# Kernel optimization log

Measured on AMD Instinct MI355X. Metric: run time of the kernel, lower is better.

The kernel has to match this reference:

```python
import jax, jax.numpy as jnp
import numpy as np

B, L, C = 4, 16384, 512   # batch, tokens (128x128 grid), dim
NH, WS = 8, 8             # num_heads, window grid (ws)
HD = C // NH              # head_dim = 64


def setup_inputs() -> dict:
    key = jax.random.key(0)
    k1, k2, k3, k4, k5 = jax.random.split(key, 5)
    return {
        "q":   jax.random.normal(k1, (B, L, C), dtype=jnp.float32),
        "kv":  jax.random.normal(k2, (B, L, C), dtype=jnp.float32),
        "Wq":  jax.random.normal(k3, (C, C), dtype=jnp.float32) * 0.02,
        "Wkv": jax.random.normal(k4, (C, 2 * C), dtype=jnp.float32) * 0.02,
        "Wfc": jax.random.normal(k5, (C, C), dtype=jnp.float32) * 0.02,
    }


def reference(q, kv, Wq, Wkv, Wfc):
    Bq, Lq, Cd = q.shape
    Lkv = kv.shape[1]
    nh, hd, ws = NH, Cd // NH, WS
    scale = hd ** (-0.5)
    hw_q = int(round(Lq ** 0.5))   # 128
    hw_k = int(round(Lkv ** 0.5))
    sq, sk = hw_q // ws, hw_k // ws  # window side lengths (16)

    qp = q @ Wq                                   # [B, Lq, C]
    kvp = (kv @ Wkv).reshape(Bq, Lkv, 2, Cd)
    k, v = kvp[:, :, 0], kvp[:, :, 1]             # [B, Lkv, C]

    def window(x, s):
        # [B, hw, hw, C] -> [B, ws*ws windows, heads, s*s tokens, hd]
        x = x.reshape(Bq, ws, s, ws, s, Cd).transpose(0, 1, 3, 2, 4, 5)
        x = x.reshape(Bq, ws * ws, s * s, nh, hd)
        return x.transpose(0, 1, 3, 2, 4)

    qw = window(qp, sq)   # [B, W, H, sq*sq, hd]
    kw = window(k, sk)    # [B, W, H, sk*sk, hd]
    vw = window(v, sk)

    attn = jnp.einsum('bwhqd,bwhkd->bwhqk', qw, kw) * scale
    attn = jax.nn.softmax(attn, axis=-1)
    o = jnp.einsum('bwhqk,bwhkd->bwhqd', attn, vw)  # [B, W, H, sq*sq, hd]

    # inverse window partition
    o = o.transpose(0, 1, 3, 2, 4).reshape(Bq, ws, ws, sq, sq, Cd)
    o = o.transpose(0, 1, 3, 2, 4, 5).reshape(Bq, Lq, Cd)
    return o @ Wfc
```

## Files before the change

### kernel.cpp

```cpp
#include <hip/hip_runtime.h>
#include <stdint.h>

#define BB 4
#define LL 16384
#define CC 512
#define MM (BB * LL)

typedef unsigned short u16;
typedef __bf16 bf16x8 __attribute__((ext_vector_type(8)));
typedef float f32x4 __attribute__((ext_vector_type(4)));
typedef u16 u16x8 __attribute__((ext_vector_type(8)));
typedef u16 u16x4 __attribute__((ext_vector_type(4)));

__device__ __forceinline__ u16 f2bf(float f) {
  union { float f; uint32_t u; } c; c.f = f;
  return (u16)((c.u + 0x7fffu + ((c.u >> 16) & 1u)) >> 16);
}

__device__ __forceinline__ void gl_lds16(const void* g, void* l) {
  __builtin_amdgcn_global_load_lds((const __attribute__((address_space(1))) void*)g,
                                   (__attribute__((address_space(3))) void*)l,
                                   16, 0, 0);
}

__global__ void cvt_kernel(const float* __restrict__ in, u16* __restrict__ out, int n4) {
  for (int i = blockIdx.x * blockDim.x + threadIdx.x; i < n4; i += gridDim.x * blockDim.x) {
    float4 v = reinterpret_cast<const float4*>(in)[i];
    u16x4 o;
    o[0] = f2bf(v.x); o[1] = f2bf(v.y); o[2] = f2bf(v.z); o[3] = f2bf(v.w);
    reinterpret_cast<u16x4*>(out)[i] = o;
  }
}

__global__ void tcvt_kernel(const float* __restrict__ W, u16* __restrict__ Wt, int K, int N) {
  int idx = blockIdx.x * blockDim.x + threadIdx.x;
  if (idx >= K * N) return;
  int n = idx / K, k = idx % K;
  Wt[idx] = f2bf(W[k * N + n]);
}

template <bool OUT_F32>
__global__ __launch_bounds__(512, 2) void gemm256(const u16* __restrict__ A,
                                                  const u16* __restrict__ Bt,
                                                  void* __restrict__ Cp,
                                                  int M, int N, int K) {
  __shared__ __align__(16) u16 Al[2][16384];
  __shared__ __align__(16) u16 Bl[2][16384];
  const int nbn = N >> 8;
  const int nwg = gridDim.x;
  const int bid0 = blockIdx.x;
  const int cpx = nwg >> 3;
  const int bid = (bid0 & 7) * cpx + (bid0 >> 3);
  const int bm = bid / nbn, bn = bid % nbn;
  const size_t row0 = (size_t)bm << 8, col0 = (size_t)bn << 8;
  const int tid = threadIdx.x, lane = tid & 63;
  const int wv = tid >> 6, wm = wv >> 2, wn = wv & 3;
  const int ro = lane & 15, g4 = lane >> 4;
  const int NT = K >> 6;

  const int ci0 = tid, ci1 = tid + 512;
  const int r0 = ci0 >> 3, g0 = (ci0 & 7) ^ (r0 & 7);
  const int r1 = ci1 >> 3, g1 = (ci1 & 7) ^ (r1 & 7);

  auto stageA = [&](int half, int kt, u16* L) {
    gl_lds16(A + (row0 + half * 128 + r0) * (size_t)K + kt * 64 + g0 * 8, L + half * 8192 + ci0 * 8);
    gl_lds16(A + (row0 + half * 128 + r1) * (size_t)K + kt * 64 + g1 * 8, L + half * 8192 + ci1 * 8);
  };
  auto stageB = [&](int half, int kt, u16* L) {
    gl_lds16(Bt + (col0 + half * 128 + r0) * (size_t)K + kt * 64 + g0 * 8, L + half * 8192 + ci0 * 8);
    gl_lds16(Bt + (col0 + half * 128 + r1) * (size_t)K + kt * 64 + g1 * 8, L + half * 8192 + ci1 * 8);
  };

  const int aB = (wm * 128 + ro) * 64;
  const int bB = (wn * 64 + ro) * 64;
  const int sw0 = (g4 ^ (ro & 7)) * 8;
  const int sw1 = ((g4 + 4) ^ (ro & 7)) * 8;

  auto ldf = [&](const u16* p) { return *reinterpret_cast<const bf16x8*>(p); };

  f32x4 acc[8][4] = {};

  stageA(0, 0, Al[0]); stageA(1, 0, Al[0]); stageB(0, 0, Bl[0]); stageB(1, 0, Bl[0]);
  stageB(0, 1, Bl[1]); stageB(1, 1, Bl[1]);
  asm volatile("s_waitcnt vmcnt(4)" ::: "memory");
  __builtin_amdgcn_s_barrier();

  for (int t = 0; t < NT; t += 2) {
#pragma unroll
    for (int half = 0; half < 2; ++half) {
      const int u = t + half;
      u16* LA = Al[half];
      u16* LB = Bl[half];
      u16* LAn = Al[half ^ 1];
      const bool stA = (u + 1) < NT;
      const bool stB = (u + 2) < NT;
      bf16x8 bfr[4][2], af[2][2];

#pragma unroll
      for (int n = 0; n < 4; ++n) {
        bfr[n][0] = ldf(LB + bB + n * 1024 + sw0);
        bfr[n][1] = ldf(LB + bB + n * 1024 + sw1);
      }
      af[0][0] = ldf(LA + aB + sw0);        af[0][1] = ldf(LA + aB + sw1);
      af[1][0] = ldf(LA + aB + 1024 + sw0); af[1][1] = ldf(LA + aB + 1024 + sw1);
      if (stA) stageA(0, u + 1, LAn);
      __builtin_amdgcn_s_barrier();
      asm volatile("s_waitcnt lgkmcnt(0)" ::: "memory");
      __builtin_amdgcn_sched_barrier(0);
      __builtin_amdgcn_s_setprio(1);
#pragma unroll
      for (int m = 0; m < 2; ++m)
#pragma unroll
        for (int n = 0; n < 4; ++n) {
          acc[m][n] = __builtin_amdgcn_mfma_f32_16x16x32_bf16(af[m][0], bfr[n][0], acc[m][n], 0, 0, 0);
          acc[m][n] = __builtin_amdgcn_mfma_f32_16x16x32_bf16(af[m][1], bfr[n][1], acc[m][n], 0, 0, 0);
        }
      __builtin_amdgcn_s_setprio(0);
      __builtin_amdgcn_s_barrier();

#pragma unroll
      for (int ph = 1; ph < 4; ++ph) {
        af[0][0] = ldf(LA + aB + (2 * ph) * 1024 + sw0);
        af[0][1] = ldf(LA + aB + (2 * ph) * 1024 + sw1);
        af[1][0] = ldf(LA + aB + (2 * ph + 1) * 1024 + sw0);
        af[1][1] = ldf(LA + aB + (2 * ph + 1) * 1024 + sw1);
        if (ph == 1) { if (stA) stageA(1, u + 1, LAn); }
        else if (ph == 2) { if (stB) stageB(0, u + 2, LB); }
        else { if (stB) stageB(1, u + 2, LB); }
        __builtin_amdgcn_s_barrier();
        asm volatile("s_waitcnt lgkmcnt(0)" ::: "memory");
        __builtin_amdgcn_sched_barrier(0);
        __builtin_amdgcn_s_setprio(1);
#pragma unroll
        for (int m = 0; m < 2; ++m)
#pragma unroll
          for (int n = 0; n < 4; ++n) {
            acc[2 * ph + m][n] =
                __builtin_amdgcn_mfma_f32_16x16x32_bf16(af[m][0], bfr[n][0], acc[2 * ph + m][n], 0, 0, 0);
            acc[2 * ph + m][n] =
                __builtin_amdgcn_mfma_f32_16x16x32_bf16(af[m][1], bfr[n][1], acc[2 * ph + m][n], 0, 0, 0);
          }
        __builtin_amdgcn_s_setprio(0);
        if (ph == 3) {
          if (stB) asm volatile("s_waitcnt vmcnt(4)" ::: "memory");
          else     asm volatile("s_waitcnt vmcnt(0)" ::: "memory");
        }
        __builtin_amdgcn_s_barrier();
      }
    }
  }

#pragma unroll
  for (int m = 0; m < 8; ++m)
#pragma unroll
    for (int n = 0; n < 4; ++n)
#pragma unroll
      for (int j = 0; j < 4; ++j) {
        size_t r = row0 + wm * 128 + m * 16 + g4 * 4 + j;
        size_t c = col0 + wn * 64 + n * 16 + ro;
        if (OUT_F32)
          reinterpret_cast<float*>(Cp)[r * N + c] = acc[m][n][j];
        else
          reinterpret_cast<u16*>(Cp)[r * N + c] = f2bf(acc[m][n][j]);
      }
}

__global__ __launch_bounds__(512, 2) void attn_kernel(const u16* __restrict__ qp,
                                                      const u16* __restrict__ kvp,
                                                      u16* __restrict__ o) {
  __shared__ __align__(16) u16 Kl[256 * 72];
  __shared__ __align__(16) u16 Vt[64 * 264];
  __shared__ __align__(16) u16 Pl[8 * 16 * 264];
  const int bid = blockIdx.x;
  const int h = bid & 7, w = (bid >> 3) & 63, b = bid >> 9;
  const int w1 = w >> 3, w2 = w & 7;
  const int tid = threadIdx.x, lane = tid & 63, wv = tid >> 6;

  auto lrow = [&](int t) { return (w1 * 16 + (t >> 4)) * 128 + w2 * 16 + (t & 15); };

  {
    const int t = tid >> 1, half = tid & 1;
    const size_t base = ((size_t)(b * LL + lrow(t))) * 1024 + h * 64 + half * 32;
    const u16* kr = kvp + base;
    const u16* vr = kvp + base + 512;
#pragma unroll
    for (int c = 0; c < 4; ++c) {
      u16x8 kx = *reinterpret_cast<const u16x8*>(kr + c * 8);
      *reinterpret_cast<u16x8*>(&Kl[t * 72 + half * 32 + c * 8]) = kx;
    }
#pragma unroll
    for (int c = 0; c < 4; ++c) {
      u16x8 vx = *reinterpret_cast<const u16x8*>(vr + c * 8);
#pragma unroll
      for (int e = 0; e < 8; ++e) Vt[(half * 32 + c * 8 + e) * 264 + t] = vx[e];
    }
  }
  __syncthreads();

  const int ro = lane & 15;
  const int g4 = lane >> 4;
  const float scale = 0.125f;
  const int pbase = wv * 16 * 264;

#pragma unroll
  for (int rt = 0; rt < 2; ++rt) {
    const int tq = 32 * wv + 16 * rt + ro;
    const size_t qbase = ((size_t)(b * LL + lrow(tq))) * 512 + h * 64 + g4 * 8;
    const bf16x8 qf0 = *reinterpret_cast<const bf16x8*>(qp + qbase);
    const bf16x8 qf1 = *reinterpret_cast<const bf16x8*>(qp + qbase + 32);

    f32x4 sa[16] = {};
#pragma unroll
    for (int ct = 0; ct < 16; ++ct) {
      bf16x8 kf0 = *reinterpret_cast<const bf16x8*>(&Kl[(16 * ct + ro) * 72 + g4 * 8]);
      bf16x8 kf1 = *reinterpret_cast<const bf16x8*>(&Kl[(16 * ct + ro) * 72 + 32 + g4 * 8]);
      sa[ct] = __builtin_amdgcn_mfma_f32_16x16x32_bf16(qf0, kf0, sa[ct], 0, 0, 0);
      sa[ct] = __builtin_amdgcn_mfma_f32_16x16x32_bf16(qf1, kf1, sa[ct], 0, 0, 0);
    }

#pragma unroll
    for (int j = 0; j < 4; ++j) {
      float m = -1e30f;
#pragma unroll
      for (int ct = 0; ct < 16; ++ct) m = fmaxf(m, sa[ct][j]);
      m = fmaxf(m, __shfl_xor(m, 1));
      m = fmaxf(m, __shfl_xor(m, 2));
      m = fmaxf(m, __shfl_xor(m, 4));
      m = fmaxf(m, __shfl_xor(m, 8));
      m *= scale;
      float s = 0.f;
#pragma unroll
      for (int ct = 0; ct < 16; ++ct) {
        float p = __expf(sa[ct][j] * scale - m);
        sa[ct][j] = p;
        s += p;
      }
      s += __shfl_xor(s, 1);
      s += __shfl_xor(s, 2);
      s += __shfl_xor(s, 4);
      s += __shfl_xor(s, 8);
      float inv = 1.f / s;
#pragma unroll
      for (int ct = 0; ct < 16; ++ct)
        Pl[pbase + (g4 * 4 + j) * 264 + 16 * ct + ro] = f2bf(sa[ct][j] * inv);
    }

    f32x4 oacc[4] = {};
#pragma unroll
    for (int ks = 0; ks < 8; ++ks) {
      bf16x8 pf = *reinterpret_cast<const bf16x8*>(&Pl[pbase + ro * 264 + ks * 32 + g4 * 8]);
#pragma unroll
      for (int cd = 0; cd < 4; ++cd) {
        bf16x8 vf = *reinterpret_cast<const bf16x8*>(&Vt[(16 * cd + ro) * 264 + ks * 32 + g4 * 8]);
        oacc[cd] = __builtin_amdgcn_mfma_f32_16x16x32_bf16(pf, vf, oacc[cd], 0, 0, 0);
      }
    }

#pragma unroll
    for (int cd = 0; cd < 4; ++cd)
#pragma unroll
      for (int j = 0; j < 4; ++j) {
        int t = 32 * wv + 16 * rt + g4 * 4 + j;
        int d = 16 * cd + ro;
        o[((size_t)(b * LL + lrow(t))) * 512 + h * 64 + d] = f2bf(oacc[cd][j]);
      }
  }
}

extern "C" void kernel_launch(void* const* d_in, const int* in_sizes, int n_in,
                              void* d_out, int out_size, void* d_ws, size_t ws_size,
                              hipStream_t stream) {
  const float* q = (const float*)d_in[0];
  const float* kv = (const float*)d_in[1];
  const float* Wq = (const float*)d_in[2];
  const float* Wkv = (const float*)d_in[3];
  const float* Wfc = (const float*)d_in[4];
  float* out = (float*)d_out;
  char* ws = (char*)d_ws;

  u16* q_bf  = (u16*)(ws + 0);
  u16* kv_bf = (u16*)(ws + 67108864);
  u16* qp    = (u16*)(ws + 134217728);
  u16* kvp   = (u16*)(ws + 201326592);
  u16* Wq_t  = (u16*)(ws + 335544320);
  u16* Wkv_t = (u16*)(ws + 336068608);
  u16* Wfc_t = (u16*)(ws + 337117184);
  u16* o_buf = q_bf;

  const int n4 = MM * CC / 4;
  cvt_kernel<<<2048, 256, 0, stream>>>(q, q_bf, n4);
  cvt_kernel<<<2048, 256, 0, stream>>>(kv, kv_bf, n4);
  tcvt_kernel<<<(CC * CC + 255) / 256, 256, 0, stream>>>(Wq, Wq_t, CC, CC);
  tcvt_kernel<<<(CC * 2 * CC + 255) / 256, 256, 0, stream>>>(Wkv, Wkv_t, CC, 2 * CC);
  tcvt_kernel<<<(CC * CC + 255) / 256, 256, 0, stream>>>(Wfc, Wfc_t, CC, CC);

  gemm256<false><<<(MM / 256) * (CC / 256), 512, 0, stream>>>(q_bf, Wq_t, qp, MM, CC, CC);
  gemm256<false><<<(MM / 256) * (2 * CC / 256), 512, 0, stream>>>(kv_bf, Wkv_t, kvp, MM, 2 * CC, CC);

  attn_kernel<<<BB * 64 * 8, 512, 0, stream>>>(qp, kvp, o_buf);

  gemm256<true><<<(MM / 256) * (CC / 256), 512, 0, stream>>>(o_buf, Wfc_t, out, MM, CC, CC);
}
```

Before: 404.8 us.

## Cut attention LDS use, read K from global, merge conversion kernels

The attention kernel drops its shared-memory K tile and loads K fragments straight from global memory. It also stages the softmax probabilities in two half-width chunks so the P buffer shrinks, and raises launch bounds to 4 blocks per CU to allow more occupancy. Separately, the two input conversion kernels and the three weight transpose kernels are each merged into one launch, and f2bf switches to the hardware bf16 conversion builtin. The risk is more global and L2 traffic for K reads, which are no longer shared across waves, plus register pressure under the tighter launch bound.

```diff
diff --git a/kernel.cpp b/kernel.cpp
--- a/kernel.cpp
+++ b/kernel.cpp
@@ -13,8 +13,7 @@
 typedef u16 u16x4 __attribute__((ext_vector_type(4)));
 
 __device__ __forceinline__ u16 f2bf(float f) {
-  union { float f; uint32_t u; } c; c.f = f;
-  return (u16)((c.u + 0x7fffu + ((c.u >> 16) & 1u)) >> 16);
+  return __builtin_bit_cast(u16, (__bf16)f);
 }
 
 __device__ __forceinline__ void gl_lds16(const void* g, void* l) {
@@ -23,20 +22,29 @@
                                    16, 0, 0);
 }
 
-__global__ void cvt_kernel(const float* __restrict__ in, u16* __restrict__ out, int n4) {
-  for (int i = blockIdx.x * blockDim.x + threadIdx.x; i < n4; i += gridDim.x * blockDim.x) {
-    float4 v = reinterpret_cast<const float4*>(in)[i];
+__global__ void cvt2_kernel(const float* __restrict__ q, const float* __restrict__ kv,
+                            u16* __restrict__ qo, u16* __restrict__ kvo, int n4) {
+  for (int i = blockIdx.x * blockDim.x + threadIdx.x; i < 2 * n4; i += gridDim.x * blockDim.x) {
+    const float* src = (i < n4) ? q : kv;
+    u16* dst = (i < n4) ? qo : kvo;
+    int k = (i < n4) ? i : i - n4;
+    float4 v = reinterpret_cast<const float4*>(src)[k];
     u16x4 o;
     o[0] = f2bf(v.x); o[1] = f2bf(v.y); o[2] = f2bf(v.z); o[3] = f2bf(v.w);
-    reinterpret_cast<u16x4*>(out)[i] = o;
+    reinterpret_cast<u16x4*>(dst)[k] = o;
   }
 }
 
-__global__ void tcvt_kernel(const float* __restrict__ W, u16* __restrict__ Wt, int K, int N) {
+__global__ void tcvt3_kernel(const float* __restrict__ Wq, const float* __restrict__ Wkv,
+                             const float* __restrict__ Wfc, u16* __restrict__ Wq_t,
+                             u16* __restrict__ Wkv_t, u16* __restrict__ Wfc_t) {
   int idx = blockIdx.x * blockDim.x + threadIdx.x;
-  if (idx >= K * N) return;
-  int n = idx / K, k = idx % K;
-  Wt[idx] = f2bf(W[k * N + n]);
+  const float* W; u16* Wt; int N, li;
+  if (idx < 262144)      { W = Wq;  Wt = Wq_t;  N = 512;  li = idx; }
+  else if (idx < 786432) { W = Wkv; Wt = Wkv_t; N = 1024; li = idx - 262144; }
+  else                   { W = Wfc; Wt = Wfc_t; N = 512;  li = idx - 786432; }
+  int n = li / 512, k = li % 512;
+  Wt[li] = f2bf(W[k * N + n]);
 }
 
 template <bool OUT_F32>
@@ -165,12 +173,11 @@
       }
 }
 
-__global__ __launch_bounds__(512, 2) void attn_kernel(const u16* __restrict__ qp,
+__global__ __launch_bounds__(512, 4) void attn_kernel(const u16* __restrict__ qp,
                                                       const u16* __restrict__ kvp,
                                                       u16* __restrict__ o) {
-  __shared__ __align__(16) u16 Kl[256 * 72];
   __shared__ __align__(16) u16 Vt[64 * 264];
-  __shared__ __align__(16) u16 Pl[8 * 16 * 264];
+  __shared__ __align__(16) u16 Pl[8][16 * 136];
   const int bid = blockIdx.x;
   const int h = bid & 7, w = (bid >> 3) & 63, b = bid >> 9;
   const int w1 = w >> 3, w2 = w & 7;
@@ -181,13 +188,7 @@
   {
     const int t = tid >> 1, half = tid & 1;
     const size_t base = ((size_t)(b * LL + lrow(t))) * 1024 + h * 64 + half * 32;
-    const u16* kr = kvp + base;
     const u16* vr = kvp + base + 512;
-#pragma unroll
-    for (int c = 0; c < 4; ++c) {
-      u16x8 kx = *reinterpret_cast<const u16x8*>(kr + c * 8);
-      *reinterpret_cast<u16x8*>(&Kl[t * 72 + half * 32 + c * 8]) = kx;
-    }
 #pragma unroll
     for (int c = 0; c < 4; ++c) {
       u16x8 vx = *reinterpret_cast<const u16x8*>(vr + c * 8);
@@ -200,7 +201,9 @@
   const int ro = lane & 15;
   const int g4 = lane >> 4;
   const float scale = 0.125f;
-  const int pbase = wv * 16 * 264;
+  u16* PW = &Pl[wv][0];
+
+  const u16* kp = kvp + ((size_t)(b * LL) + w1 * 2048 + w2 * 16 + ro) * 1024 + h * 64 + g4 * 8;
 
 #pragma unroll
   for (int rt = 0; rt < 2; ++rt) {
@@ -212,8 +215,8 @@
     f32x4 sa[16] = {};
 #pragma unroll
     for (int ct = 0; ct < 16; ++ct) {
-      bf16x8 kf0 = *reinterpret_cast<const bf16x8*>(&Kl[(16 * ct + ro) * 72 + g4 * 8]);
-      bf16x8 kf1 = *reinterpret_cast<const bf16x8*>(&Kl[(16 * ct + ro) * 72 + 32 + g4 * 8]);
+      bf16x8 kf0 = *reinterpret_cast<const bf16x8*>(kp + ct * 131072);
+      bf16x8 kf1 = *reinterpret_cast<const bf16x8*>(kp + ct * 131072 + 32);
       sa[ct] = __builtin_amdgcn_mfma_f32_16x16x32_bf16(qf0, kf0, sa[ct], 0, 0, 0);
       sa[ct] = __builtin_amdgcn_mfma_f32_16x16x32_bf16(qf1, kf1, sa[ct], 0, 0, 0);
     }
@@ -241,18 +244,26 @@
       s += __shfl_xor(s, 8);
       float inv = 1.f / s;
 #pragma unroll
-      for (int ct = 0; ct < 16; ++ct)
-        Pl[pbase + (g4 * 4 + j) * 264 + 16 * ct + ro] = f2bf(sa[ct][j] * inv);
+      for (int ct = 0; ct < 16; ++ct) sa[ct][j] *= inv;
     }
 
     f32x4 oacc[4] = {};
 #pragma unroll
-    for (int ks = 0; ks < 8; ++ks) {
-      bf16x8 pf = *reinterpret_cast<const bf16x8*>(&Pl[pbase + ro * 264 + ks * 32 + g4 * 8]);
-#pragma unroll
-      for (int cd = 0; cd < 4; ++cd) {
-        bf16x8 vf = *reinterpret_cast<const bf16x8*>(&Vt[(16 * cd + ro) * 264 + ks * 32 + g4 * 8]);
-        oacc[cd] = __builtin_amdgcn_mfma_f32_16x16x32_bf16(pf, vf, oacc[cd], 0, 0, 0);
+    for (int kh = 0; kh < 2; ++kh) {
+#pragma unroll
+      for (int j = 0; j < 4; ++j)
+#pragma unroll
+        for (int c = 0; c < 8; ++c)
+          PW[(g4 * 4 + j) * 136 + 16 * c + ro] = f2bf(sa[kh * 8 + c][j]);
+#pragma unroll
+      for (int ks = 0; ks < 4; ++ks) {
+        bf16x8 pf = *reinterpret_cast<const bf16x8*>(&PW[ro * 136 + ks * 32 + g4 * 8]);
+#pragma unroll
+        for (int cd = 0; cd < 4; ++cd) {
+          bf16x8 vf = *reinterpret_cast<const bf16x8*>(
+              &Vt[(16 * cd + ro) * 264 + (kh * 4 + ks) * 32 + g4 * 8]);
+          oacc[cd] = __builtin_amdgcn_mfma_f32_16x16x32_bf16(pf, vf, oacc[cd], 0, 0, 0);
+        }
       }
     }
 
@@ -288,11 +299,8 @@
   u16* o_buf = q_bf;
 
   const int n4 = MM * CC / 4;
-  cvt_kernel<<<2048, 256, 0, stream>>>(q, q_bf, n4);
-  cvt_kernel<<<2048, 256, 0, stream>>>(kv, kv_bf, n4);
-  tcvt_kernel<<<(CC * CC + 255) / 256, 256, 0, stream>>>(Wq, Wq_t, CC, CC);
-  tcvt_kernel<<<(CC * 2 * CC + 255) / 256, 256, 0, stream>>>(Wkv, Wkv_t, CC, 2 * CC);
-  tcvt_kernel<<<(CC * CC + 255) / 256, 256, 0, stream>>>(Wfc, Wfc_t, CC, CC);
+  cvt2_kernel<<<4096, 256, 0, stream>>>(q, kv, q_bf, kv_bf, n4);
+  tcvt3_kernel<<<4096, 256, 0, stream>>>(Wq, Wkv, Wfc, Wq_t, Wkv_t, Wfc_t);
 
   gemm256<false><<<(MM / 256) * (CC / 256), 512, 0, stream>>>(q_bf, Wq_t, qp, MM, CC, CC);
   gemm256<false><<<(MM / 256) * (2 * CC / 256), 512, 0, stream>>>(kv_bf, Wkv_t, kvp, MM, 2 * CC, CC);
```

Measured after the change: 453.1 us. 11.9% more time.
